# Performance work log

Hardware: AMD Instinct MI355X
Metric: run time of the kernel (lower is better)

The kernel has to match this reference:

```python
import jax, jax.numpy as jnp
import numpy as np

H = 16      # attention_head_num
DH = 64     # attention_head_size
D = H * DH  # out_dim = 1024


def setup_inputs() -> dict:
    key = jax.random.key(0)
    ks = jax.random.split(key, 9)
    s = 1.0 / np.sqrt(D)
    x = jax.random.normal(ks[0], (2, 2048, D), dtype=jnp.float32)
    Wq = jax.random.uniform(ks[1], (D, D), jnp.float32, -s, s)
    bq = jax.random.uniform(ks[2], (D,), jnp.float32, -s, s)
    Wk = jax.random.uniform(ks[3], (D, D), jnp.float32, -s, s)
    bk = jax.random.uniform(ks[4], (D,), jnp.float32, -s, s)
    Wv = jax.random.uniform(ks[5], (D, D), jnp.float32, -s, s)
    bv = jax.random.uniform(ks[6], (D,), jnp.float32, -s, s)
    Wo = jax.random.uniform(ks[7], (D, D), jnp.float32, -s, s)
    bo = jax.random.uniform(ks[8], (D,), jnp.float32, -s, s)
    return {"x": x, "Wq": Wq, "bq": bq, "Wk": Wk, "bk": bk,
            "Wv": Wv, "bv": bv, "Wo": Wo, "bo": bo}


def reference(x, Wq, bq, Wk, bk, Wv, bv, Wo, bo):
    B, S, _ = x.shape
    # projections (nn.Linear: x @ W^T + b)
    q = (x @ Wq.T + bq).reshape(B, S, H, DH).transpose(0, 2, 1, 3)  # [B,H,S,Dh]
    k = (x @ Wk.T + bk).reshape(B, S, H, DH).transpose(0, 2, 1, 3)
    v = (x @ Wv.T + bv).reshape(B, S, H, DH).transpose(0, 2, 1, 3)
    scores = jnp.einsum('bhqd,bhkd->bhqk', q, k) / jnp.sqrt(jnp.float32(DH))
    probs = jax.nn.softmax(scores, axis=-1)  # dropout is identity in eval mode
    ctx = jnp.einsum('bhqk,bhkd->bhqd', probs, v)
    ctx = ctx.transpose(0, 2, 1, 3).reshape(B, S, D)
    return ctx @ Wo.T + bo
```

## Files before the change

kernel.cpp:

```cpp
#include <hip/hip_runtime.h>
#include <hip/hip_bf16.h>
#include <stdint.h>

typedef __attribute__((ext_vector_type(8))) short bf16x8;
typedef __attribute__((ext_vector_type(8))) unsigned short u16x8;
typedef __attribute__((ext_vector_type(4))) unsigned short u16x4;
typedef __attribute__((ext_vector_type(4))) float f32x4;

constexpr int NB  = 2;
constexpr int NS  = 2048;
constexpr int NH  = 16;
constexpr int NDH = 64;
constexpr int ND  = 1024;

static __device__ __forceinline__ unsigned short bfbits(float f) {
    union { float f; uint32_t u; } v; v.f = f;
    uint32_t u = v.u + 0x7FFFu + ((v.u >> 16) & 1u);
    return (unsigned short)(u >> 16);
}

static __device__ __forceinline__ float fexp2(float x) {
#if __has_builtin(__builtin_amdgcn_exp2f)
    return __builtin_amdgcn_exp2f(x);
#else
    return exp2f(x);
#endif
}

static __device__ __forceinline__ void gl_lds16(const void* g, void* l) {
    __builtin_amdgcn_global_load_lds(
        (const __attribute__((address_space(1))) unsigned int*)g,
        (__attribute__((address_space(3))) unsigned int*)l, 16, 0, 0);
}

__global__ __launch_bounds__(256)
void cvt_kernel(const float* __restrict__ x,  const float* __restrict__ wq,
                const float* __restrict__ wk, const float* __restrict__ wv,
                const float* __restrict__ wo,
                unsigned short* __restrict__ xb,  unsigned short* __restrict__ wqb,
                unsigned short* __restrict__ wkb, unsigned short* __restrict__ wvb,
                unsigned short* __restrict__ wob)
{
    const int b = blockIdx.x;
    const float* s; unsigned short* d; int off;
    if      (b < 2048) { s = x;  d = xb;  off = b; }
    else if (b < 2560) { s = wq; d = wqb; off = b - 2048; }
    else if (b < 3072) { s = wk; d = wkb; off = b - 2560; }
    else if (b < 3584) { s = wv; d = wvb; off = b - 3072; }
    else               { s = wo; d = wob; off = b - 3584; }
    const size_t idx = ((size_t)off * 256 + threadIdx.x) * 8;
    float4 f0 = *(const float4*)&s[idx];
    float4 f1 = *(const float4*)&s[idx + 4];
    u16x8 o;
    o[0] = bfbits(f0.x); o[1] = bfbits(f0.y); o[2] = bfbits(f0.z); o[3] = bfbits(f0.w);
    o[4] = bfbits(f1.x); o[5] = bfbits(f1.y); o[6] = bfbits(f1.z); o[7] = bfbits(f1.w);
    *(u16x8*)&d[idx] = o;
}

__global__ __launch_bounds__(256, 2)
void qkv_kernel(const unsigned short* __restrict__ xb,
                const unsigned short* __restrict__ wqb,
                const unsigned short* __restrict__ wkb,
                const unsigned short* __restrict__ wvb,
                const float* __restrict__ bq, const float* __restrict__ bk,
                const float* __restrict__ bv,
                unsigned short* __restrict__ qbuf,
                unsigned short* __restrict__ kbuf,
                unsigned short* __restrict__ vtbuf)
{
    __shared__ unsigned short As[128 * 64];
    __shared__ unsigned short Bs[128 * 64];
    __shared__ unsigned short Tt[128][136];

    const int fid = blockIdx.x + blockIdx.y * 24;
    const int xcd = fid & 7, idx = fid >> 3;
    const int bx  = idx >> 2;
    const int by  = xcd * 4 + (idx & 3);

    const int m0  = by * 128;
    const int jg0 = bx * 128;
    const int proj = jg0 >> 10;
    const int n0   = jg0 & 1023;
    const unsigned short* W = (proj == 0) ? wqb : (proj == 1) ? wkb : wvb;
    const float* bias       = (proj == 0) ? bq  : (proj == 1) ? bk  : bv;

    const int tid = threadIdx.x, lane = tid & 63, wid = tid >> 6;
    const int wm = wid >> 1, wn = wid & 1;
    const int l15 = lane & 15, g = lane >> 4;

    const f32x4 fzero = {0.f, 0.f, 0.f, 0.f};
    f32x4 acc[4][4];
#pragma unroll
    for (int i = 0; i < 4; i++)
#pragma unroll
        for (int j = 0; j < 4; j++) acc[i][j] = fzero;

    const int srow = tid >> 3;
    const int scb  = ((tid & 7) * 16) ^ ((srow & 7) << 4);
    const char* asrc = (const char*)xb + (size_t)(m0 + srow) * 2048 + scb;
    const char* bsrc = (const char*)W  + (size_t)(n0 + srow) * 2048 + scb;
    char* adst = (char*)As + tid * 16;
    char* bdst = (char*)Bs + tid * 16;
    const int xm = (l15 & 7) << 4;

    for (int k0 = 0; k0 < 1024; k0 += 64) {
#pragma unroll
        for (int i = 0; i < 4; i++) {
            gl_lds16(asrc + (size_t)i * 32 * 2048 + k0 * 2, adst + i * 4096);
            gl_lds16(bsrc + (size_t)i * 32 * 2048 + k0 * 2, bdst + i * 4096);
        }
        __syncthreads();
#pragma unroll
        for (int kk = 0; kk < 2; kk++) {
            bf16x8 af[4], bfr[4];
#pragma unroll
            for (int i = 0; i < 4; i++) {
                const int row = wm * 64 + i * 16 + l15;
                af[i] = *(const bf16x8*)((const char*)As + row * 128 + ((kk * 64 + g * 16) ^ xm));
            }
#pragma unroll
            for (int j = 0; j < 4; j++) {
                const int row = wn * 64 + j * 16 + l15;
                bfr[j] = *(const bf16x8*)((const char*)Bs + row * 128 + ((kk * 64 + g * 16) ^ xm));
            }
#pragma unroll
            for (int i = 0; i < 4; i++)
#pragma unroll
                for (int j = 0; j < 4; j++)
                    acc[i][j] = __builtin_amdgcn_mfma_f32_16x16x32_bf16(af[i], bfr[j], acc[i][j], 0, 0, 0);
        }
        __syncthreads();
    }

    if (proj < 2) {
        unsigned short* qk_out = (proj == 0) ? qbuf : kbuf;
        const float qs = (proj == 0) ? 0.18033688f : 1.0f;
#pragma unroll
        for (int j = 0; j < 4; j++) {
            const int col = n0 + wn * 64 + j * 16 + l15;
            const float bsv = bias[col];
            const int h = col >> 6, dh = col & 63;
#pragma unroll
            for (int i = 0; i < 4; i++)
#pragma unroll
                for (int r = 0; r < 4; r++) {
                    const int row = m0 + wm * 64 + i * 16 + g * 4 + r;
                    const int b_ = row >> 11, s_ = row & (NS - 1);
                    qk_out[((size_t)((b_ * NH + h) * NS + s_)) * NDH + dh] =
                        bfbits((acc[i][j][r] + bsv) * qs);
                }
        }
    } else {
#pragma unroll
        for (int j = 0; j < 4; j++) {
            const int cl = wn * 64 + j * 16 + l15;
            const float bsv = bias[n0 + cl];
#pragma unroll
            for (int i = 0; i < 4; i++) {
                u16x4 w4;
#pragma unroll
                for (int r = 0; r < 4; r++) w4[r] = bfbits(acc[i][j][r] + bsv);
                *(u16x4*)&Tt[cl][wm * 64 + i * 16 + g * 4] = w4;
            }
        }
        __syncthreads();
        const int b_ = m0 >> 11, s0 = m0 & (NS - 1);
        const int h0 = n0 >> 6;
#pragma unroll
        for (int it = 0; it < 8; it++) {
            const int c = wid * 32 + it * 4 + g;
            u16x8 v8 = *(const u16x8*)&Tt[c][l15 * 8];
            const size_t row = (size_t)(b_ * NH + h0 + (c >> 6)) * NDH + (c & 63);
            *(u16x8*)&vtbuf[row * NS + s0 + l15 * 8] = v8;
        }
    }
}

__global__ __launch_bounds__(256, 4)
void attn_kernel(const unsigned short* __restrict__ qbuf,
                 const unsigned short* __restrict__ kbuf,
                 const unsigned short* __restrict__ vtbuf,
                 unsigned short* __restrict__ ctxbuf)
{
    __shared__ unsigned short Ks[2][64 * 64];
    __shared__ unsigned short Vs[2][64 * 64];

    const int fid  = blockIdx.x + blockIdx.y * 32;
    const int nid  = (fid & 7) * 128 + (fid >> 3);
    const int bx   = nid & 31, bh = nid >> 5;
    const int q0   = bx * 64;

    const int tid = threadIdx.x, lane = tid & 63, wid = tid >> 6;
    const int l15 = lane & 15, g = lane >> 4;

    const unsigned short* qb = qbuf  + (size_t)bh * NS * NDH;
    const unsigned short* kb = kbuf  + (size_t)bh * NS * NDH;
    const unsigned short* vb = vtbuf + (size_t)bh * NDH * NS;

    const int qrow = q0 + wid * 16 + l15;
    const bf16x8 qf0 = *(const bf16x8*)&qb[(size_t)qrow * NDH + g * 8];
    const bf16x8 qf1 = *(const bf16x8*)&qb[(size_t)qrow * NDH + 32 + g * 8];

    const short oneb = (short)0x3F80;
    const bf16x8 ones = {oneb, oneb, oneb, oneb, oneb, oneb, oneb, oneb};

    const f32x4 fzero = {0.f, 0.f, 0.f, 0.f};
    f32x4 acc[4];
#pragma unroll
    for (int d = 0; d < 4; d++) acc[d] = fzero;
    f32x4 acc_l = fzero;

    const int o = tid * 16;
    const int srow = o >> 7;
    const int scb  = (o & 127) ^ ((srow & 7) << 4);
    const char* ksrc  = (const char*)kb + srow * 128 + scb;
    const char* ksrc2 = (const char*)kb + (srow + 32) * 128 + (( (o & 127) ^ (((srow + 32) & 7) << 4)));
    const char* vsrc  = (const char*)vb + (size_t)srow * (NS * 2) + scb;
    const char* vsrc2 = (const char*)vb + (size_t)(srow + 32) * (NS * 2) + ((o & 127) ^ (((srow + 32) & 7) << 4));
    char* kbase = (char*)Ks;
    char* vbase = (char*)Vs;
    const int xm = (l15 & 7) << 4;

    auto STAGE = [&](int b, int t_) {
        gl_lds16(ksrc  + (size_t)t_ * 8192, kbase + b * 8192 + o);
        gl_lds16(ksrc2 + (size_t)t_ * 8192, kbase + b * 8192 + 4096 + o);
        gl_lds16(vsrc  + (size_t)t_ * 128,  vbase + b * 8192 + o);
        gl_lds16(vsrc2 + (size_t)t_ * 128,  vbase + b * 8192 + 4096 + o);
    };

    STAGE(0, 0);
    asm volatile("s_waitcnt vmcnt(0)" ::: "memory");
    __builtin_amdgcn_s_barrier();
    asm volatile("" ::: "memory");

    for (int t = 0; t < 32; t++) {
        const int cb = t & 1;
        if (t < 31) STAGE(cb ^ 1, t + 1);

        const char* ksb = kbase + cb * 8192;
        const char* vsb = vbase + cb * 8192;

        f32x4 sv[4];
#pragma unroll
        for (int kt = 0; kt < 4; kt++) {
            const char* rb = ksb + (kt * 16 + l15) * 128;
            bf16x8 kf0 = *(const bf16x8*)(rb + ((g * 16) ^ xm));
            bf16x8 kf1 = *(const bf16x8*)(rb + ((64 + g * 16) ^ xm));
            f32x4 s4 = fzero;
            s4 = __builtin_amdgcn_mfma_f32_16x16x32_bf16(kf0, qf0, s4, 0, 0, 0);
            s4 = __builtin_amdgcn_mfma_f32_16x16x32_bf16(kf1, qf1, s4, 0, 0, 0);
            sv[kt] = s4;
        }

#pragma unroll
        for (int kt = 0; kt < 4; kt++)
#pragma unroll
            for (int r = 0; r < 4; r++)
                sv[kt][r] = fexp2(sv[kt][r]);

        bf16x8 pf[2];
#pragma unroll
        for (int f = 0; f < 2; f++) {
            const int kt0 = f * 2;
            union { __hip_bfloat162 h2; uint32_t u; } c0, c1, c2, c3;
            float2 p01 = { sv[kt0][0], sv[kt0][1] };
            float2 p23 = { sv[kt0][2], sv[kt0][3] };
            float2 p45 = { sv[kt0 + 1][0], sv[kt0 + 1][1] };
            float2 p67 = { sv[kt0 + 1][2], sv[kt0 + 1][3] };
            c0.h2 = __float22bfloat162_rn(p01);
            c1.h2 = __float22bfloat162_rn(p23);
            c2.h2 = __float22bfloat162_rn(p45);
            c3.h2 = __float22bfloat162_rn(p67);
            uint32_t a0 = c0.u, a1 = c1.u, b0 = c2.u, b1 = c3.u;
            asm("v_permlane32_swap_b32 %0, %1" : "+v"(a0), "+v"(b0));
            asm("v_permlane32_swap_b32 %0, %1" : "+v"(a1), "+v"(b1));
            asm("v_permlane16_swap_b32 %0, %1" : "+v"(a0), "+v"(b0));
            asm("v_permlane16_swap_b32 %0, %1" : "+v"(a1), "+v"(b1));
            union { uint32_t w[4]; bf16x8 fr; } r_;
            r_.w[0] = a0; r_.w[1] = a1; r_.w[2] = b0; r_.w[3] = b1;
            pf[f] = r_.fr;
        }

        acc_l = __builtin_amdgcn_mfma_f32_16x16x32_bf16(pf[0], ones, acc_l, 0, 0, 0);
        acc_l = __builtin_amdgcn_mfma_f32_16x16x32_bf16(pf[1], ones, acc_l, 0, 0, 0);
#pragma unroll
        for (int d = 0; d < 4; d++) {
            const char* rb = vsb + (d * 16 + l15) * 128;
            bf16x8 vf0 = *(const bf16x8*)(rb + ((g * 16) ^ xm));
            bf16x8 vf1 = *(const bf16x8*)(rb + ((64 + g * 16) ^ xm));
            acc[d] = __builtin_amdgcn_mfma_f32_16x16x32_bf16(pf[0], vf0, acc[d], 0, 0, 0);
            acc[d] = __builtin_amdgcn_mfma_f32_16x16x32_bf16(pf[1], vf1, acc[d], 0, 0, 0);
        }

        asm volatile("s_waitcnt vmcnt(0)" ::: "memory");
        __builtin_amdgcn_s_barrier();
        asm volatile("" ::: "memory");
    }

    const int b_ = bh >> 4, h_ = bh & 15;
#pragma unroll
    for (int r = 0; r < 4; r++) {
        const float inv = 1.f / acc_l[r];
        const int sq = q0 + wid * 16 + g * 4 + r;
        const size_t base = ((size_t)(b_ * NS + sq)) * ND + h_ * NDH;
#pragma unroll
        for (int d = 0; d < 4; d++)
            ctxbuf[base + d * 16 + l15] = bfbits(acc[d][r] * inv);
    }
}

__global__ __launch_bounds__(256, 2)
void out_kernel(const unsigned short* __restrict__ ctx,
                const unsigned short* __restrict__ wob,
                const float* __restrict__ bo,
                float* __restrict__ out)
{
    __shared__ unsigned short As[128 * 64];
    __shared__ unsigned short Bs[128 * 64];

    const int n0 = blockIdx.x * 128;
    const int m0 = blockIdx.y * 128;
    const int tid = threadIdx.x, lane = tid & 63, wid = tid >> 6;
    const int wm = wid >> 1, wn = wid & 1;
    const int l15 = lane & 15, g = lane >> 4;

    const f32x4 fzero = {0.f, 0.f, 0.f, 0.f};
    f32x4 acc[4][4];
#pragma unroll
    for (int i = 0; i < 4; i++)
#pragma unroll
        for (int j = 0; j < 4; j++) acc[i][j] = fzero;

    const int srow = tid >> 3;
    const int scb  = ((tid & 7) * 16) ^ ((srow & 7) << 4);
    const char* asrc = (const char*)ctx + (size_t)(m0 + srow) * 2048 + scb;
    const char* bsrc = (const char*)wob + (size_t)(n0 + srow) * 2048 + scb;
    char* adst = (char*)As + tid * 16;
    char* bdst = (char*)Bs + tid * 16;
    const int xm = (l15 & 7) << 4;

    for (int k0 = 0; k0 < 1024; k0 += 64) {
#pragma unroll
        for (int i = 0; i < 4; i++) {
            gl_lds16(asrc + (size_t)i * 32 * 2048 + k0 * 2, adst + i * 4096);
            gl_lds16(bsrc + (size_t)i * 32 * 2048 + k0 * 2, bdst + i * 4096);
        }
        __syncthreads();
#pragma unroll
        for (int kk = 0; kk < 2; kk++) {
            bf16x8 af[4], bfr[4];
#pragma unroll
            for (int i = 0; i < 4; i++) {
                const int row = wm * 64 + i * 16 + l15;
                af[i] = *(const bf16x8*)((const char*)As + row * 128 + ((kk * 64 + g * 16) ^ xm));
            }
#pragma unroll
            for (int j = 0; j < 4; j++) {
                const int row = wn * 64 + j * 16 + l15;
                bfr[j] = *(const bf16x8*)((const char*)Bs + row * 128 + ((kk * 64 + g * 16) ^ xm));
            }
#pragma unroll
            for (int i = 0; i < 4; i++)
#pragma unroll
                for (int j = 0; j < 4; j++)
                    acc[i][j] = __builtin_amdgcn_mfma_f32_16x16x32_bf16(af[i], bfr[j], acc[i][j], 0, 0, 0);
        }
        __syncthreads();
    }

#pragma unroll
    for (int j = 0; j < 4; j++) {
        const int col = n0 + wn * 64 + j * 16 + l15;
        const float bsv = bo[col];
#pragma unroll
        for (int i = 0; i < 4; i++)
#pragma unroll
            for (int r = 0; r < 4; r++) {
                const int row = m0 + wm * 64 + i * 16 + g * 4 + r;
                out[(size_t)row * ND + col] = acc[i][j][r] + bsv;
            }
    }
}

extern "C" void kernel_launch(void* const* d_in, const int* in_sizes, int n_in,
                              void* d_out, int out_size, void* d_ws, size_t ws_size,
                              hipStream_t stream) {
    const float* x  = (const float*)d_in[0];
    const float* Wq = (const float*)d_in[1];
    const float* bq = (const float*)d_in[2];
    const float* Wk = (const float*)d_in[3];
    const float* bk = (const float*)d_in[4];
    const float* Wv = (const float*)d_in[5];
    const float* bv = (const float*)d_in[6];
    const float* Wo = (const float*)d_in[7];
    const float* bo = (const float*)d_in[8];
    float* out = (float*)d_out;

    const size_t qk_elems = (size_t)NB * NH * NS * NDH;
    const size_t w_elems  = (size_t)ND * ND;
    unsigned short* qbuf   = (unsigned short*)d_ws;
    unsigned short* kbuf   = qbuf + qk_elems;
    unsigned short* vtbuf  = kbuf + qk_elems;
    unsigned short* ctxbuf = vtbuf + qk_elems;
    unsigned short* xb     = ctxbuf + qk_elems;
    unsigned short* wqb    = xb + qk_elems;
    unsigned short* wkb    = wqb + w_elems;
    unsigned short* wvb    = wkb + w_elems;
    unsigned short* wob    = wvb + w_elems;

    cvt_kernel<<<4096, 256, 0, stream>>>(x, Wq, Wk, Wv, Wo, xb, wqb, wkb, wvb, wob);
    qkv_kernel<<<dim3(24, 32), 256, 0, stream>>>(xb, wqb, wkb, wvb, bq, bk, bv,
                                                 qbuf, kbuf, vtbuf);
    attn_kernel<<<dim3(32, 32), 256, 0, stream>>>(qbuf, kbuf, vtbuf, ctxbuf);
    out_kernel<<<dim3(8, 32), 256, 0, stream>>>(ctxbuf, wob, bo, out);
}
```

Baseline: 119.1 us.

## Split attention waves across key halves with two query groups each

Each wave now handles 32 query rows (two 16-row groups) over half of each 64-key tile, instead of 16 query rows over the full tile. Each K/V fragment loaded from shared memory then feeds two MFMAs, roughly halving LDS reads per MFMA. The two key-half partial accumulators and row sums are combined through shared memory at the end. This costs more accumulator registers and an extra barrier plus an LDS reduction in the epilogue.

Measured after the change: 114.0 us. -4.3%, faster.

```diff
diff --git a/kernel.cpp b/kernel.cpp
--- a/kernel.cpp
+++ b/kernel.cpp
@@ -182,8 +182,9 @@
                  const unsigned short* __restrict__ vtbuf,
                  unsigned short* __restrict__ ctxbuf)
 {
-    __shared__ unsigned short Ks[2][64 * 64];
-    __shared__ unsigned short Vs[2][64 * 64];
+    __shared__ char smem[32768];
+    char* kbase = smem;
+    char* vbase = smem + 16384;
 
     const int fid  = blockIdx.x + blockIdx.y * 32;
     const int nid  = (fid & 7) * 128 + (fid >> 3);
@@ -192,33 +193,38 @@
 
     const int tid = threadIdx.x, lane = tid & 63, wid = tid >> 6;
     const int l15 = lane & 15, g = lane >> 4;
+    const int qh = wid >> 1, ks = wid & 1;
 
     const unsigned short* qb = qbuf  + (size_t)bh * NS * NDH;
     const unsigned short* kb = kbuf  + (size_t)bh * NS * NDH;
     const unsigned short* vb = vtbuf + (size_t)bh * NDH * NS;
 
-    const int qrow = q0 + wid * 16 + l15;
-    const bf16x8 qf0 = *(const bf16x8*)&qb[(size_t)qrow * NDH + g * 8];
-    const bf16x8 qf1 = *(const bf16x8*)&qb[(size_t)qrow * NDH + 32 + g * 8];
+    bf16x8 qf[2][2];
+#pragma unroll
+    for (int qg = 0; qg < 2; qg++) {
+        const int qrow = q0 + qh * 32 + qg * 16 + l15;
+        qf[qg][0] = *(const bf16x8*)&qb[(size_t)qrow * NDH + g * 8];
+        qf[qg][1] = *(const bf16x8*)&qb[(size_t)qrow * NDH + 32 + g * 8];
+    }
 
     const short oneb = (short)0x3F80;
     const bf16x8 ones = {oneb, oneb, oneb, oneb, oneb, oneb, oneb, oneb};
 
     const f32x4 fzero = {0.f, 0.f, 0.f, 0.f};
-    f32x4 acc[4];
-#pragma unroll
-    for (int d = 0; d < 4; d++) acc[d] = fzero;
-    f32x4 acc_l = fzero;
+    f32x4 acc[2][4];
+#pragma unroll
+    for (int qg = 0; qg < 2; qg++)
+#pragma unroll
+        for (int d = 0; d < 4; d++) acc[qg][d] = fzero;
+    f32x4 acc_l[2] = {fzero, fzero};
 
     const int o = tid * 16;
     const int srow = o >> 7;
     const int scb  = (o & 127) ^ ((srow & 7) << 4);
     const char* ksrc  = (const char*)kb + srow * 128 + scb;
-    const char* ksrc2 = (const char*)kb + (srow + 32) * 128 + (( (o & 127) ^ (((srow + 32) & 7) << 4)));
+    const char* ksrc2 = (const char*)kb + (srow + 32) * 128 + scb;
     const char* vsrc  = (const char*)vb + (size_t)srow * (NS * 2) + scb;
-    const char* vsrc2 = (const char*)vb + (size_t)(srow + 32) * (NS * 2) + ((o & 127) ^ (((srow + 32) & 7) << 4));
-    char* kbase = (char*)Ks;
-    char* vbase = (char*)Vs;
+    const char* vsrc2 = (const char*)vb + (size_t)(srow + 32) * (NS * 2) + scb;
     const int xm = (l15 & 7) << 4;
 
     auto STAGE = [&](int b, int t_) {
@@ -240,33 +246,38 @@
         const char* ksb = kbase + cb * 8192;
         const char* vsb = vbase + cb * 8192;
 
-        f32x4 sv[4];
-#pragma unroll
-        for (int kt = 0; kt < 4; kt++) {
-            const char* rb = ksb + (kt * 16 + l15) * 128;
+        f32x4 sv[2][2];
+#pragma unroll
+        for (int kt = 0; kt < 2; kt++) {
+            const int row = ks * 32 + kt * 16 + l15;
+            const char* rb = ksb + row * 128;
             bf16x8 kf0 = *(const bf16x8*)(rb + ((g * 16) ^ xm));
             bf16x8 kf1 = *(const bf16x8*)(rb + ((64 + g * 16) ^ xm));
-            f32x4 s4 = fzero;
-            s4 = __builtin_amdgcn_mfma_f32_16x16x32_bf16(kf0, qf0, s4, 0, 0, 0);
-            s4 = __builtin_amdgcn_mfma_f32_16x16x32_bf16(kf1, qf1, s4, 0, 0, 0);
-            sv[kt] = s4;
-        }
-
-#pragma unroll
-        for (int kt = 0; kt < 4; kt++)
-#pragma unroll
-            for (int r = 0; r < 4; r++)
-                sv[kt][r] = fexp2(sv[kt][r]);
+#pragma unroll
+            for (int qg = 0; qg < 2; qg++) {
+                f32x4 s4 = fzero;
+                s4 = __builtin_amdgcn_mfma_f32_16x16x32_bf16(kf0, qf[qg][0], s4, 0, 0, 0);
+                s4 = __builtin_amdgcn_mfma_f32_16x16x32_bf16(kf1, qf[qg][1], s4, 0, 0, 0);
+                sv[qg][kt] = s4;
+            }
+        }
+
+#pragma unroll
+        for (int qg = 0; qg < 2; qg++)
+#pragma unroll
+            for (int kt = 0; kt < 2; kt++)
+#pragma unroll
+                for (int r = 0; r < 4; r++)
+                    sv[qg][kt][r] = fexp2(sv[qg][kt][r]);
 
         bf16x8 pf[2];
 #pragma unroll
-        for (int f = 0; f < 2; f++) {
-            const int kt0 = f * 2;
+        for (int qg = 0; qg < 2; qg++) {
             union { __hip_bfloat162 h2; uint32_t u; } c0, c1, c2, c3;
-            float2 p01 = { sv[kt0][0], sv[kt0][1] };
-            float2 p23 = { sv[kt0][2], sv[kt0][3] };
-            float2 p45 = { sv[kt0 + 1][0], sv[kt0 + 1][1] };
-            float2 p67 = { sv[kt0 + 1][2], sv[kt0 + 1][3] };
+            float2 p01 = { sv[qg][0][0], sv[qg][0][1] };
+            float2 p23 = { sv[qg][0][2], sv[qg][0][3] };
+            float2 p45 = { sv[qg][1][0], sv[qg][1][1] };
+            float2 p67 = { sv[qg][1][2], sv[qg][1][3] };
             c0.h2 = __float22bfloat162_rn(p01);
             c1.h2 = __float22bfloat162_rn(p23);
             c2.h2 = __float22bfloat162_rn(p45);
@@ -278,18 +289,20 @@
             asm("v_permlane16_swap_b32 %0, %1" : "+v"(a1), "+v"(b1));
             union { uint32_t w[4]; bf16x8 fr; } r_;
             r_.w[0] = a0; r_.w[1] = a1; r_.w[2] = b0; r_.w[3] = b1;
-            pf[f] = r_.fr;
-        }
-
-        acc_l = __builtin_amdgcn_mfma_f32_16x16x32_bf16(pf[0], ones, acc_l, 0, 0, 0);
-        acc_l = __builtin_amdgcn_mfma_f32_16x16x32_bf16(pf[1], ones, acc_l, 0, 0, 0);
+            pf[qg] = r_.fr;
+        }
+
+#pragma unroll
+        for (int qg = 0; qg < 2; qg++)
+            acc_l[qg] = __builtin_amdgcn_mfma_f32_16x16x32_bf16(pf[qg], ones, acc_l[qg], 0, 0, 0);
 #pragma unroll
         for (int d = 0; d < 4; d++) {
-            const char* rb = vsb + (d * 16 + l15) * 128;
-            bf16x8 vf0 = *(const bf16x8*)(rb + ((g * 16) ^ xm));
-            bf16x8 vf1 = *(const bf16x8*)(rb + ((64 + g * 16) ^ xm));
-            acc[d] = __builtin_amdgcn_mfma_f32_16x16x32_bf16(pf[0], vf0, acc[d], 0, 0, 0);
-            acc[d] = __builtin_amdgcn_mfma_f32_16x16x32_bf16(pf[1], vf1, acc[d], 0, 0, 0);
+            const int row = d * 16 + l15;
+            const char* rb = vsb + row * 128;
+            bf16x8 vf = *(const bf16x8*)(rb + ((ks * 64 + g * 16) ^ xm));
+#pragma unroll
+            for (int qg = 0; qg < 2; qg++)
+                acc[qg][d] = __builtin_amdgcn_mfma_f32_16x16x32_bf16(pf[qg], vf, acc[qg][d], 0, 0, 0);
         }
 
         asm volatile("s_waitcnt vmcnt(0)" ::: "memory");
@@ -297,15 +310,38 @@
         asm volatile("" ::: "memory");
     }
 
-    const int b_ = bh >> 4, h_ = bh & 15;
-#pragma unroll
-    for (int r = 0; r < 4; r++) {
-        const float inv = 1.f / acc_l[r];
-        const int sq = q0 + wid * 16 + g * 4 + r;
-        const size_t base = ((size_t)(b_ * NS + sq)) * ND + h_ * NDH;
-#pragma unroll
-        for (int d = 0; d < 4; d++)
-            ctxbuf[base + d * 16 + l15] = bfbits(acc[d][r] * inv);
+    if (ks == 1) {
+#pragma unroll
+        for (int qg = 0; qg < 2; qg++)
+#pragma unroll
+            for (int d = 0; d < 4; d++)
+                *(f32x4*)(smem + qh * 10240 + ((qg * 4 + d) * 64 + lane) * 16) = acc[qg][d];
+#pragma unroll
+        for (int qg = 0; qg < 2; qg++)
+            *(f32x4*)(smem + qh * 10240 + 8192 + (qg * 64 + lane) * 16) = acc_l[qg];
+    }
+    __syncthreads();
+    if (ks == 0) {
+#pragma unroll
+        for (int qg = 0; qg < 2; qg++) {
+#pragma unroll
+            for (int d = 0; d < 4; d++)
+                acc[qg][d] += *(const f32x4*)(smem + qh * 10240 + ((qg * 4 + d) * 64 + lane) * 16);
+            acc_l[qg] += *(const f32x4*)(smem + qh * 10240 + 8192 + (qg * 64 + lane) * 16);
+        }
+
+        const int b_ = bh >> 4, h_ = bh & 15;
+#pragma unroll
+        for (int qg = 0; qg < 2; qg++)
+#pragma unroll
+            for (int r = 0; r < 4; r++) {
+                const float inv = 1.f / acc_l[qg][r];
+                const int sq = q0 + qh * 32 + qg * 16 + g * 4 + r;
+                const size_t base = ((size_t)(b_ * NS + sq)) * ND + h_ * NDH;
+#pragma unroll
+                for (int d = 0; d < 4; d++)
+                    ctxbuf[base + d * 16 + l15] = bfbits(acc[qg][d][r] * inv);
+            }
     }
 }
 
```
